# Kernel optimization log

Hardware: AMD Instinct MI355X
Metric: run time of the kernel (lower is better)

Reference implementation:

```python
import jax, jax.numpy as jnp
import numpy as np

B, N_IN, N_OUT, K, V = 8, 2048, 2048, 64, 64


def setup_inputs() -> dict:
    key = jax.random.key(0)
    k1, k2, k3 = jax.random.split(key, 3)
    return {
        "key": jax.random.normal(k1, (B, N_IN, 1, K), dtype=jnp.float32),
        "query": jax.random.normal(k2, (B, 1, N_OUT, K), dtype=jnp.float32),
        "value": jax.random.normal(k3, (B, N_IN, V), dtype=jnp.float32),
    }


def reference(key, query, value):
    ks = key.shape[-1]
    # sum(key * query, 3) / sqrt(key_size)  ==  batched GEMM over key_size
    # weights: [B, n_inputs, n_outputs]
    weights = jnp.einsum("bik,bok->bio", key[:, :, 0, :], query[:, 0, :, :]) / jnp.sqrt(
        jnp.asarray(ks, dtype=key.dtype)
    )
    weights = jax.nn.softmax(weights, axis=1)  # softmax over n_inputs
    # sum(weights[...,None] * value[:,:,None,:], 1) -> [B, n_outputs, value_size]
    vals = jnp.einsum("bio,biv->bov", weights, value)
    # row-wise L2 normalize each [value_size] vector
    vals = vals / (jnp.linalg.norm(vals, axis=-1, keepdims=True) + 1e-12)
    values = jnp.swapaxes(vals, 1, 2)  # [B, value_size, n_outputs]
    return values, weights
```

## Files before the change

kernel.cpp:

```cpp
#include <hip/hip_runtime.h>

#define NB 8
#define NN 2048
#define KK 64
#define VV 64
#define SCALE 0.18033688011112043f

typedef __bf16 bfrag  __attribute__((ext_vector_type(8)));
typedef __bf16 bf16x4 __attribute__((ext_vector_type(4)));
typedef float  f32x4  __attribute__((ext_vector_type(4)));

__device__ __forceinline__ int swz(int row, int colByte) {
  return row * 128 + (colByte ^ ((row & 7) << 4));
}

__device__ __forceinline__ bfrag lds_frag(const unsigned short* base, int row, int colByte) {
  return *reinterpret_cast<const bfrag*>(reinterpret_cast<const char*>(base) + swz(row, colByte));
}

__device__ __forceinline__ bfrag g_frag(const float* __restrict__ g) {
  const float4* p = reinterpret_cast<const float4*>(g);
  float4 x = p[0], y = p[1];
  bfrag r;
  r[0] = (__bf16)x.x; r[1] = (__bf16)x.y; r[2] = (__bf16)x.z; r[3] = (__bf16)x.w;
  r[4] = (__bf16)y.x; r[5] = (__bf16)y.y; r[6] = (__bf16)y.z; r[7] = (__bf16)y.w;
  return r;
}

struct KS { float4 f[4]; };
__device__ __forceinline__ void k_load(KS& s, const float* __restrict__ g) {
  const float4* p = reinterpret_cast<const float4*>(g);
  s.f[0] = p[0]; s.f[1] = p[1]; s.f[2] = p[2]; s.f[3] = p[3];
}
__device__ __forceinline__ void k_write(const KS& s, unsigned short* lds, int row, int colByte) {
  const float* f = reinterpret_cast<const float*>(&s.f[0]);
  bfrag a, b;
#pragma unroll
  for (int j = 0; j < 8; ++j) a[j] = (__bf16)f[j];
#pragma unroll
  for (int j = 0; j < 8; ++j) b[j] = (__bf16)f[8 + j];
  *reinterpret_cast<bfrag*>(reinterpret_cast<char*>(lds) + swz(row, colByte)) = a;
  *reinterpret_cast<bfrag*>(reinterpret_cast<char*>(lds) + swz(row, colByte + 16)) = b;
}

struct VS { float4 f[4]; };
__device__ __forceinline__ void v_load(VS& s, const float* __restrict__ g) {
  const float4* p = reinterpret_cast<const float4*>(g);
  s.f[0] = p[0]; s.f[1] = p[1];
  const float4* q = reinterpret_cast<const float4*>(g + VV);
  s.f[2] = q[0]; s.f[3] = q[1];
}
__device__ __forceinline__ void v_write(const VS& s, unsigned short* lds, int il, int v0) {
  const float* lo = reinterpret_cast<const float*>(&s.f[0]);
  const float* hi = reinterpret_cast<const float*>(&s.f[2]);
#pragma unroll
  for (int j = 0; j < 8; ++j) {
    __bf16 two[2] = { (__bf16)lo[j], (__bf16)hi[j] };
    *reinterpret_cast<unsigned*>(reinterpret_cast<char*>(lds) + swz(v0 + j, il * 2)) =
        *reinterpret_cast<unsigned*>(two);
  }
}

#define CHUNK 512
#define IT 64
#define K1STEPS (CHUNK / IT)
#define SCR_STRIDE 4160

__global__ void __launch_bounds__(256) attn_pass1(
    const float* __restrict__ key, const float* __restrict__ query,
    const float* __restrict__ value, float* __restrict__ scratch)
{
  __shared__ __align__(16) unsigned short Kt[IT * KK];
  __shared__ __align__(16) unsigned short Vt[VV * IT];
  __shared__ __align__(16) unsigned short Et[64 * IT];
  __shared__ float Red[4][64];

  const int tid  = threadIdx.x;
  const int lane = tid & 63;
  const int wv   = tid >> 6;
  const int l15  = lane & 15;
  const int l4   = lane >> 4;

  const int b    = blockIdx.x & 7;
  const int rest = blockIdx.x >> 3;
  const int ot   = rest & 31;
  const int ci   = rest >> 5;
  const int o0   = ot * 64;
  const int ib0  = ci * CHUNK;

  const float* Kg = key   + (size_t)b * NN * KK;
  const float* Qg = query + (size_t)b * NN * KK;
  const float* Vg = value + (size_t)b * NN * VV;
  float* scr = scratch + (size_t)((b * 32 + ot) * 4 + ci) * SCR_STRIDE;

  const int krow = tid >> 2;
  const int kel  = (tid & 3) * 16;
  const int kcb  = (tid & 3) * 32;
  const int vil  = (tid & 31) * 2;
  const int vv0  = (tid >> 5) * 8;

  bfrag qb0[4], qb1[4];
#pragma unroll
  for (int s = 0; s < 4; ++s) {
    const float* qr = Qg + (size_t)(o0 + s * 16 + l15) * KK;
    qb0[s] = g_frag(qr + l4 * 8);
    qb1[s] = g_frag(qr + 32 + l4 * 8);
  }

  KS ks; VS vs;
  k_load(ks, Kg + (size_t)(ib0 + krow) * KK + kel);
  v_load(vs, Vg + (size_t)(ib0 + vil) * VV + vv0);
  k_write(ks, Kt, krow, kcb);
  v_write(vs, Vt, vil, vv0);
  __syncthreads();

  f32x4 uacc[4];
  float Dacc[4] = {0.f, 0.f, 0.f, 0.f};
#pragma unroll
  for (int s = 0; s < 4; ++s) { f32x4 z = {0.f, 0.f, 0.f, 0.f}; uacc[s] = z; }

  for (int t = 0; t < K1STEPS; ++t) {
    if (t + 1 < K1STEPS) {
      k_load(ks, Kg + (size_t)(ib0 + (t + 1) * IT + krow) * KK + kel);
      v_load(vs, Vg + (size_t)(ib0 + (t + 1) * IT + vil) * VV + vv0);
    }
    bfrag a0 = lds_frag(Kt, wv * 16 + l15, l4 * 16);
    bfrag a1 = lds_frag(Kt, wv * 16 + l15, 64 + l4 * 16);
#pragma unroll
    for (int s = 0; s < 4; ++s) {
      f32x4 z = {0.f, 0.f, 0.f, 0.f};
      z = __builtin_amdgcn_mfma_f32_16x16x32_bf16(a0, qb0[s], z, 0, 0, 0);
      z = __builtin_amdgcn_mfma_f32_16x16x32_bf16(a1, qb1[s], z, 0, 0, 0);
      f32x4 e;
#pragma unroll
      for (int r = 0; r < 4; ++r) e[r] = exp2f(z[r] * SCALE);
      Dacc[s] += e[0] + e[1] + e[2] + e[3];
      bf16x4 pk;
#pragma unroll
      for (int r = 0; r < 4; ++r) pk[r] = (__bf16)e[r];
      *reinterpret_cast<bf16x4*>(reinterpret_cast<char*>(Et) +
                                 swz(s * 16 + l15, wv * 32 + l4 * 8)) = pk;
    }
    __syncthreads();
    if (t + 1 < K1STEPS) k_write(ks, Kt, krow, kcb);
    bfrag va0 = lds_frag(Vt, wv * 16 + l15, l4 * 16);
    bfrag va1 = lds_frag(Vt, wv * 16 + l15, 64 + l4 * 16);
#pragma unroll
    for (int s = 0; s < 4; ++s) {
      bfrag e0 = lds_frag(Et, s * 16 + l15, l4 * 16);
      bfrag e1 = lds_frag(Et, s * 16 + l15, 64 + l4 * 16);
      uacc[s] = __builtin_amdgcn_mfma_f32_16x16x32_bf16(va0, e0, uacc[s], 0, 0, 0);
      uacc[s] = __builtin_amdgcn_mfma_f32_16x16x32_bf16(va1, e1, uacc[s], 0, 0, 0);
    }
    __syncthreads();
    if (t + 1 < K1STEPS) v_write(vs, Vt, vil, vv0);
  }

#pragma unroll
  for (int s = 0; s < 4; ++s)
#pragma unroll
    for (int r = 0; r < 4; ++r)
      scr[(wv * 16 + l4 * 4 + r) * 64 + s * 16 + l15] = uacc[s][r];

#pragma unroll
  for (int s = 0; s < 4; ++s) {
    float d = Dacc[s];
    d += __shfl_xor(d, 16, 64);
    d += __shfl_xor(d, 32, 64);
    if (lane < 16) Red[wv][s * 16 + lane] = d;
  }
  __syncthreads();
  if (tid < 64)
    scr[4096 + tid] = Red[0][tid] + Red[1][tid] + Red[2][tid] + Red[3][tid];
}

__global__ void __launch_bounds__(512) attn_reduce(
    const float* __restrict__ scratch, float* __restrict__ outV,
    float* __restrict__ invD)
{
  __shared__ float R2[8][64];
  __shared__ float Nn[64];

  const int tid = threadIdx.x;
  const int b   = blockIdx.x & 7;
  const int ot  = blockIdx.x >> 3;
  const float* base = scratch + (size_t)(b * 32 + ot) * 4 * SCR_STRIDE;

  const int ol = tid & 63;
  const int vg = tid >> 6;

  float u[8];
#pragma unroll
  for (int j = 0; j < 8; ++j) u[j] = 0.f;
#pragma unroll
  for (int c = 0; c < 4; ++c) {
    const float* p = base + c * SCR_STRIDE;
#pragma unroll
    for (int j = 0; j < 8; ++j) u[j] += p[(vg + 8 * j) * 64 + ol];
  }
  float ssq = 0.f;
#pragma unroll
  for (int j = 0; j < 8; ++j) ssq += u[j] * u[j];
  R2[vg][ol] = ssq;
  __syncthreads();
  if (tid < 64) {
    float n = 0.f;
#pragma unroll
    for (int g = 0; g < 8; ++g) n += R2[g][tid];
    Nn[tid] = 1.f / (sqrtf(n) + 1e-12f);
    float D = 0.f;
#pragma unroll
    for (int c = 0; c < 4; ++c) D += base[c * SCR_STRIDE + 4096 + tid];
    invD[b * NN + ot * 64 + tid] = 1.f / D;
  }
  __syncthreads();
  const float inn = Nn[ol];
  float* vp = outV + (size_t)b * VV * NN + ot * 64 + ol;
#pragma unroll
  for (int j = 0; j < 8; ++j)
    vp[(size_t)(vg + 8 * j) * NN] = u[j] * inn;
}

__global__ void __launch_bounds__(256) attn_weights(
    const float* __restrict__ key, const float* __restrict__ query,
    const float* __restrict__ invD, float* __restrict__ outWall)
{
  __shared__ __align__(16) unsigned short Kt2[128 * 64];

  const int tid  = threadIdx.x;
  const int lane = tid & 63;
  const int wv   = tid >> 6;
  const int l15  = lane & 15;
  const int l4   = lane >> 4;

  const int b    = blockIdx.x & 7;
  const int rest = blockIdx.x >> 3;
  const int it   = rest & 15;
  const int ot   = rest >> 4;

  const float* Kg = key   + (size_t)b * NN * KK;
  const float* Qg = query + (size_t)b * NN * KK;
  float* outW = outWall + (size_t)b * NN * NN;

  {
    const int krow = tid >> 1;
    const int half = (tid & 1);
    KS sA, sB;
    k_load(sA, Kg + (size_t)(it * 128 + krow) * KK + half * 32);
    k_load(sB, Kg + (size_t)(it * 128 + krow) * KK + half * 32 + 16);
    k_write(sA, Kt2, krow, half * 64);
    k_write(sB, Kt2, krow, half * 64 + 32);
  }

  bfrag a0[2], a1[2];
#pragma unroll
  for (int m = 0; m < 2; ++m) {
    const float* qr = Qg + (size_t)(ot * 128 + wv * 32 + m * 16 + l15) * KK;
    a0[m] = g_frag(qr + l4 * 8);
    a1[m] = g_frag(qr + 32 + l4 * 8);
  }
  f32x4 id[2];
#pragma unroll
  for (int m = 0; m < 2; ++m)
    id[m] = *reinterpret_cast<const f32x4*>(
        &invD[b * NN + ot * 128 + wv * 32 + m * 16 + l4 * 4]);
  __syncthreads();

  f32x4 acc[2][8];
#pragma unroll
  for (int m = 0; m < 2; ++m)
#pragma unroll
    for (int s = 0; s < 8; ++s) { f32x4 z = {0.f, 0.f, 0.f, 0.f}; acc[m][s] = z; }

#pragma unroll
  for (int s = 0; s < 8; ++s) {
    bfrag b0 = lds_frag(Kt2, s * 16 + l15, l4 * 16);
    bfrag b1 = lds_frag(Kt2, s * 16 + l15, 64 + l4 * 16);
#pragma unroll
    for (int m = 0; m < 2; ++m) {
      acc[m][s] = __builtin_amdgcn_mfma_f32_16x16x32_bf16(a0[m], b0, acc[m][s], 0, 0, 0);
      acc[m][s] = __builtin_amdgcn_mfma_f32_16x16x32_bf16(a1[m], b1, acc[m][s], 0, 0, 0);
    }
  }

#pragma unroll
  for (int s = 0; s < 8; ++s)
#pragma unroll
    for (int m = 0; m < 2; ++m) {
      f32x4 w;
#pragma unroll
      for (int r = 0; r < 4; ++r) w[r] = exp2f(acc[m][s][r] * SCALE) * id[m][r];
      float* wp = outW + (size_t)(it * 128 + s * 16 + l15) * NN +
                  ot * 128 + wv * 32 + m * 16 + l4 * 4;
      *reinterpret_cast<f32x4*>(wp) = w;
    }
}

extern "C" void kernel_launch(void* const* d_in, const int* in_sizes, int n_in,
                              void* d_out, int out_size, void* d_ws, size_t ws_size,
                              hipStream_t stream) {
  (void)in_sizes; (void)n_in; (void)ws_size; (void)out_size;
  const float* key   = (const float*)d_in[0];
  const float* query = (const float*)d_in[1];
  const float* value = (const float*)d_in[2];
  float* out  = (float*)d_out;
  float* outV = out;
  float* outW = out + (size_t)NB * VV * NN;
  float* invD = (float*)d_ws;
  float* scratch = outW;

  attn_pass1 <<<dim3(NB * 32 * 4), dim3(256), 0, stream>>>(key, query, value, scratch);
  attn_reduce<<<dim3(NB * 32),     dim3(512), 0, stream>>>(scratch, outV, invD);
  attn_weights<<<dim3(NB * 16 * 16), dim3(256), 0, stream>>>(key, query, invD, outW);
}
```

Baseline: 79.04 us.

## Keep softmax exps in registers and double-buffer V tiles in pass1

The first attention pass now splits its four waves into a 2x2 grid over inputs and outputs. Each wave loads its K rows directly from global memory in a permuted order, so the MFMA result layout can be reused as the B operand of the value MFMA. This removes the Et LDS round trip, drops the K LDS staging, and leaves one barrier per step by double-buffering V. The two input-half partial results are merged through LDS before writing scratch, and launch bounds request 4 blocks per SM. The trade-offs are redundant global K loads per wave and higher register pressure from more accumulators.

```diff
diff --git a/kernel.cpp b/kernel.cpp
--- a/kernel.cpp
+++ b/kernel.cpp
@@ -62,24 +62,26 @@
 }
 
 #define CHUNK 512
-#define IT 64
-#define K1STEPS (CHUNK / IT)
+#define K1STEPS (CHUNK / 64)
 #define SCR_STRIDE 4160
 
-__global__ void __launch_bounds__(256) attn_pass1(
+__global__ void __launch_bounds__(256, 4) attn_pass1(
     const float* __restrict__ key, const float* __restrict__ query,
     const float* __restrict__ value, float* __restrict__ scratch)
 {
-  __shared__ __align__(16) unsigned short Kt[IT * KK];
-  __shared__ __align__(16) unsigned short Vt[VV * IT];
-  __shared__ __align__(16) unsigned short Et[64 * IT];
-  __shared__ float Red[4][64];
+  __shared__ __align__(16) char smem[16640];
+  __shared__ float Red[4][32];
+  unsigned short* Vt0 = reinterpret_cast<unsigned short*>(smem);
+  unsigned short* Vt1 = reinterpret_cast<unsigned short*>(smem + 8192);
+  float* Ured = reinterpret_cast<float*>(smem);
 
   const int tid  = threadIdx.x;
   const int lane = tid & 63;
-  const int wv   = tid >> 6;
+  const int w    = tid >> 6;
   const int l15  = lane & 15;
   const int l4   = lane >> 4;
+  const int ihalf = w & 1;
+  const int ohalf = w >> 1;
 
   const int b    = blockIdx.x & 7;
   const int rest = blockIdx.x >> 3;
@@ -93,85 +95,116 @@
   const float* Vg = value + (size_t)b * NN * VV;
   float* scr = scratch + (size_t)((b * 32 + ot) * 4 + ci) * SCR_STRIDE;
 
-  const int krow = tid >> 2;
-  const int kel  = (tid & 3) * 16;
-  const int kcb  = (tid & 3) * 32;
-  const int vil  = (tid & 31) * 2;
-  const int vv0  = (tid >> 5) * 8;
-
-  bfrag qb0[4], qb1[4];
-#pragma unroll
-  for (int s = 0; s < 4; ++s) {
-    const float* qr = Qg + (size_t)(o0 + s * 16 + l15) * KK;
-    qb0[s] = g_frag(qr + l4 * 8);
-    qb1[s] = g_frag(qr + 32 + l4 * 8);
-  }
-
-  KS ks; VS vs;
-  k_load(ks, Kg + (size_t)(ib0 + krow) * KK + kel);
+  bfrag qb[2][2];
+#pragma unroll
+  for (int s = 0; s < 2; ++s) {
+    const float* qr = Qg + (size_t)(o0 + ohalf * 32 + s * 16 + l15) * KK;
+    qb[s][0] = g_frag(qr + l4 * 8);
+    qb[s][1] = g_frag(qr + 32 + l4 * 8);
+  }
+
+  const int iperm = (l15 & 3) + ((l15 >> 2) * 8);
+
+  const int vil = (tid & 31) * 2;
+  const int vv0 = (tid >> 5) * 8;
+
+  VS vs;
   v_load(vs, Vg + (size_t)(ib0 + vil) * VV + vv0);
-  k_write(ks, Kt, krow, kcb);
-  v_write(vs, Vt, vil, vv0);
-  __syncthreads();
-
-  f32x4 uacc[4];
-  float Dacc[4] = {0.f, 0.f, 0.f, 0.f};
-#pragma unroll
-  for (int s = 0; s < 4; ++s) { f32x4 z = {0.f, 0.f, 0.f, 0.f}; uacc[s] = z; }
+  v_write(vs, Vt0, vil, vv0);
+  __syncthreads();
+
+  f32x4 uacc[4][2];
+#pragma unroll
+  for (int vc = 0; vc < 4; ++vc)
+#pragma unroll
+    for (int s = 0; s < 2; ++s) { f32x4 z = {0.f,0.f,0.f,0.f}; uacc[vc][s] = z; }
+  float Dacc[2] = {0.f, 0.f};
 
   for (int t = 0; t < K1STEPS; ++t) {
-    if (t + 1 < K1STEPS) {
-      k_load(ks, Kg + (size_t)(ib0 + (t + 1) * IT + krow) * KK + kel);
-      v_load(vs, Vg + (size_t)(ib0 + (t + 1) * IT + vil) * VV + vv0);
+    unsigned short* Vcur = (t & 1) ? Vt1 : Vt0;
+    unsigned short* Vnxt = (t & 1) ? Vt0 : Vt1;
+    if (t + 1 < K1STEPS)
+      v_load(vs, Vg + (size_t)(ib0 + (t + 1) * 64 + vil) * VV + vv0);
+
+    const int ibase = ib0 + t * 64 + ihalf * 32;
+    const float* kr1 = Kg + (size_t)(ibase + iperm) * KK;
+    const float* kr2 = Kg + (size_t)(ibase + iperm + 4) * KK;
+    bfrag ka10 = g_frag(kr1 + l4 * 8), ka11 = g_frag(kr1 + 32 + l4 * 8);
+    bfrag ka20 = g_frag(kr2 + l4 * 8), ka21 = g_frag(kr2 + 32 + l4 * 8);
+
+    bfrag eb[2];
+#pragma unroll
+    for (int s = 0; s < 2; ++s) {
+      f32x4 z1 = {0.f,0.f,0.f,0.f}, z2 = {0.f,0.f,0.f,0.f};
+      z1 = __builtin_amdgcn_mfma_f32_16x16x32_bf16(ka10, qb[s][0], z1, 0, 0, 0);
+      z1 = __builtin_amdgcn_mfma_f32_16x16x32_bf16(ka11, qb[s][1], z1, 0, 0, 0);
+      z2 = __builtin_amdgcn_mfma_f32_16x16x32_bf16(ka20, qb[s][0], z2, 0, 0, 0);
+      z2 = __builtin_amdgcn_mfma_f32_16x16x32_bf16(ka21, qb[s][1], z2, 0, 0, 0);
+      f32x4 e1, e2;
+#pragma unroll
+      for (int r = 0; r < 4; ++r) e1[r] = exp2f(z1[r] * SCALE);
+#pragma unroll
+      for (int r = 0; r < 4; ++r) e2[r] = exp2f(z2[r] * SCALE);
+      Dacc[s] += e1[0] + e1[1] + e1[2] + e1[3] + e2[0] + e2[1] + e2[2] + e2[3];
+      bfrag e;
+#pragma unroll
+      for (int r = 0; r < 4; ++r) e[r]     = (__bf16)e1[r];
+#pragma unroll
+      for (int r = 0; r < 4; ++r) e[4 + r] = (__bf16)e2[r];
+      eb[s] = e;
     }
-    bfrag a0 = lds_frag(Kt, wv * 16 + l15, l4 * 16);
-    bfrag a1 = lds_frag(Kt, wv * 16 + l15, 64 + l4 * 16);
-#pragma unroll
-    for (int s = 0; s < 4; ++s) {
-      f32x4 z = {0.f, 0.f, 0.f, 0.f};
-      z = __builtin_amdgcn_mfma_f32_16x16x32_bf16(a0, qb0[s], z, 0, 0, 0);
-      z = __builtin_amdgcn_mfma_f32_16x16x32_bf16(a1, qb1[s], z, 0, 0, 0);
-      f32x4 e;
-#pragma unroll
-      for (int r = 0; r < 4; ++r) e[r] = exp2f(z[r] * SCALE);
-      Dacc[s] += e[0] + e[1] + e[2] + e[3];
-      bf16x4 pk;
-#pragma unroll
-      for (int r = 0; r < 4; ++r) pk[r] = (__bf16)e[r];
-      *reinterpret_cast<bf16x4*>(reinterpret_cast<char*>(Et) +
-                                 swz(s * 16 + l15, wv * 32 + l4 * 8)) = pk;
-    }
+
+    bfrag va[4];
+#pragma unroll
+    for (int vc = 0; vc < 4; ++vc)
+      va[vc] = lds_frag(Vcur, vc * 16 + l15, ihalf * 64 + l4 * 16);
+#pragma unroll
+    for (int vc = 0; vc < 4; ++vc)
+#pragma unroll
+      for (int s = 0; s < 2; ++s)
+        uacc[vc][s] = __builtin_amdgcn_mfma_f32_16x16x32_bf16(va[vc], eb[s], uacc[vc][s], 0, 0, 0);
+
+    if (t + 1 < K1STEPS) v_write(vs, Vnxt, vil, vv0);
     __syncthreads();
-    if (t + 1 < K1STEPS) k_write(ks, Kt, krow, kcb);
-    bfrag va0 = lds_frag(Vt, wv * 16 + l15, l4 * 16);
-    bfrag va1 = lds_frag(Vt, wv * 16 + l15, 64 + l4 * 16);
-#pragma unroll
-    for (int s = 0; s < 4; ++s) {
-      bfrag e0 = lds_frag(Et, s * 16 + l15, l4 * 16);
-      bfrag e1 = lds_frag(Et, s * 16 + l15, 64 + l4 * 16);
-      uacc[s] = __builtin_amdgcn_mfma_f32_16x16x32_bf16(va0, e0, uacc[s], 0, 0, 0);
-      uacc[s] = __builtin_amdgcn_mfma_f32_16x16x32_bf16(va1, e1, uacc[s], 0, 0, 0);
-    }
-    __syncthreads();
-    if (t + 1 < K1STEPS) v_write(vs, Vt, vil, vv0);
-  }
-
-#pragma unroll
-  for (int s = 0; s < 4; ++s)
-#pragma unroll
-    for (int r = 0; r < 4; ++r)
-      scr[(wv * 16 + l4 * 4 + r) * 64 + s * 16 + l15] = uacc[s][r];
-
-#pragma unroll
-  for (int s = 0; s < 4; ++s) {
+  }
+
+#pragma unroll
+  for (int s = 0; s < 2; ++s) {
     float d = Dacc[s];
     d += __shfl_xor(d, 16, 64);
     d += __shfl_xor(d, 32, 64);
-    if (lane < 16) Red[wv][s * 16 + lane] = d;
-  }
-  __syncthreads();
-  if (tid < 64)
-    scr[4096 + tid] = Red[0][tid] + Red[1][tid] + Red[2][tid] + Red[3][tid];
+    if (lane < 16) Red[w][s * 16 + lane] = d;
+  }
+
+  if (ihalf == 0) {
+#pragma unroll
+    for (int vc = 0; vc < 4; ++vc)
+#pragma unroll
+      for (int s = 0; s < 2; ++s)
+#pragma unroll
+        for (int r = 0; r < 4; ++r)
+          Ured[(vc * 16 + l4 * 4 + r) * 65 + ohalf * 32 + s * 16 + l15] = uacc[vc][s][r];
+  }
+  __syncthreads();
+  if (ihalf == 1) {
+#pragma unroll
+    for (int vc = 0; vc < 4; ++vc)
+#pragma unroll
+      for (int s = 0; s < 2; ++s)
+#pragma unroll
+        for (int r = 0; r < 4; ++r)
+          Ured[(vc * 16 + l4 * 4 + r) * 65 + ohalf * 32 + s * 16 + l15] += uacc[vc][s][r];
+  }
+  if (tid < 64) {
+    const int oh = tid >> 5, ol = tid & 31;
+    scr[4096 + tid] = Red[oh * 2][ol] + Red[oh * 2 + 1][ol];
+  }
+  __syncthreads();
+#pragma unroll
+  for (int j = 0; j < 16; ++j) {
+    const int idx = j * 256 + tid;
+    scr[idx] = Ured[(idx >> 6) * 65 + (idx & 63)];
+  }
 }
 
 __global__ void __launch_bounds__(512) attn_reduce(
@@ -270,7 +303,7 @@
 #pragma unroll
   for (int m = 0; m < 2; ++m)
 #pragma unroll
-    for (int s = 0; s < 8; ++s) { f32x4 z = {0.f, 0.f, 0.f, 0.f}; acc[m][s] = z; }
+    for (int s = 0; s < 8; ++s) { f32x4 z = {0.f,0.f,0.f,0.f}; acc[m][s] = z; }
 
 #pragma unroll
   for (int s = 0; s < 8; ++s) {
```

Result: slower. 90.37 us (+14.3%).
